# Optimization experiments

Measured on AMD Instinct MI355X. Metric: run time of the kernel, lower is better.

The kernel has to match this reference:

```python
import jax, jax.numpy as jnp
import numpy as np


def _rotate_half(t):
    t1, t2 = jnp.split(t, 2, axis=-1)
    return jnp.concatenate([-t2, t1], axis=-1)


def setup_inputs() -> dict:
    key = jax.random.key(0)
    ks = jax.random.split(key, 6)
    B, N, C, H = 4, 2048, 1024, 16
    D = C // H
    N_ROPE = N - 4  # prefix of 4 tokens skips RoPE
    return {
        "x": jax.random.normal(ks[0], (B, N, C), dtype=jnp.float32),
        "sin": jax.random.normal(ks[1], (N_ROPE, D), dtype=jnp.float32),
        "cos": jax.random.normal(ks[2], (N_ROPE, D), dtype=jnp.float32),
        "w_qkv": jax.random.normal(ks[3], (3 * C, C), dtype=jnp.float32) * (C ** -0.5),
        "w_proj": jax.random.normal(ks[4], (C, C), dtype=jnp.float32) * (C ** -0.5),
        "b_proj": jax.random.normal(ks[5], (C,), dtype=jnp.float32) * 0.02,
    }


def reference(x, sin, cos, w_qkv, w_proj, b_proj):
    B, N, C = x.shape
    H = 16
    D = C // H
    # QKV projection (no bias): [B,N,3C] -> [B,N,3,H,D]
    qkv = jnp.einsum("bnc,fc->bnf", x, w_qkv).reshape(B, N, 3, H, D)
    q, k, v = (jnp.transpose(qkv[:, :, i], (0, 2, 1, 3)) for i in range(3))  # [B,H,N,D]
    # RoPE on suffix tokens only (prefix = N - rope_len)
    prefix = N - sin.shape[-2]
    q_s, k_s = q[:, :, prefix:, :], k[:, :, prefix:, :]
    q = jnp.concatenate([q[:, :, :prefix, :], q_s * cos + _rotate_half(q_s) * sin], axis=2)
    k = jnp.concatenate([k[:, :, :prefix, :], k_s * cos + _rotate_half(k_s) * sin], axis=2)
    # Scaled dot-product attention
    scale = 1.0 / jnp.sqrt(jnp.asarray(D, dtype=q.dtype))
    attn = jax.nn.softmax(jnp.einsum("bhqd,bhkd->bhqk", q, k) * scale, axis=-1)
    o = jnp.einsum("bhqk,bhkd->bhqd", attn, v)
    o = jnp.transpose(o, (0, 2, 1, 3)).reshape(B, N, C)
    return jnp.einsum("bnc,oc->bno", o, w_proj) + b_proj
```

## Files before the change

### kernel.cpp

```cpp
#include <hip/hip_runtime.h>
#include <stdint.h>

typedef __bf16 bf16x8 __attribute__((ext_vector_type(8)));
typedef _Float16 f16x8 __attribute__((ext_vector_type(8)));
typedef float f32x4 __attribute__((ext_vector_type(4)));
typedef short s16x8 __attribute__((ext_vector_type(8)));
typedef short s16x4 __attribute__((ext_vector_type(4)));
typedef unsigned int u32x4 __attribute__((ext_vector_type(4)));

__device__ __forceinline__ unsigned short f2bf(float f) {
  unsigned u = __builtin_bit_cast(unsigned, f);
  u += 0x7fff + ((u >> 16) & 1);
  return (unsigned short)(u >> 16);
}
__device__ __forceinline__ unsigned short f2h(float f) {
  return __builtin_bit_cast(unsigned short, (_Float16)f);
}
__device__ __forceinline__ float exp2i(float x) {
  float r;
  asm("v_exp_f32 %0, %1" : "=v"(r) : "v"(x));
  return r;
}
__device__ __forceinline__ float max3f(float a, float b, float c) {
  float r;
  asm("v_max3_f32 %0, %1, %2, %3" : "=v"(r) : "v"(a), "v"(b), "v"(c));
  return r;
}
__device__ __forceinline__ unsigned cvtpkh(float lo, float hi) {
  auto r = __builtin_amdgcn_cvt_pkrtz(lo, hi);
  return __builtin_bit_cast(unsigned, r);
}

__device__ __forceinline__ void gload_lds16(const void* g, void* l) {
  __builtin_amdgcn_global_load_lds(
      (const __attribute__((address_space(1))) unsigned int*)g,
      (__attribute__((address_space(3))) unsigned int*)l, 16, 0, 0);
}

__device__ __forceinline__ f32x4 mfma_bf(bf16x8 a, bf16x8 b, f32x4 c) {
  return __builtin_amdgcn_mfma_f32_16x16x32_bf16(a, b, c, 0, 0, 0);
}
__device__ __forceinline__ f32x4 mfma_h(f16x8 a, f16x8 b, f32x4 c) {
  return __builtin_amdgcn_mfma_f32_16x16x32_f16(a, b, c, 0, 0, 0);
}
__device__ __forceinline__ bf16x8 bc8(s16x8 v) { return __builtin_bit_cast(bf16x8, v); }
__device__ __forceinline__ f16x8 hc8(s16x8 v) { return __builtin_bit_cast(f16x8, v); }

__global__ void k_cvt_all(const float* __restrict__ x, const float* __restrict__ wq,
                          const float* __restrict__ wp,
                          unsigned short* __restrict__ xb,
                          unsigned short* __restrict__ wqb,
                          unsigned short* __restrict__ wpb) {
  int i = blockIdx.x * blockDim.x + threadIdx.x;
  const float* in; unsigned short* out; int j = i;
  if (i < 2097152)        { in = x;  out = xb;  }
  else if (i < 2883584)   { in = wq; out = wqb; j = i - 2097152; }
  else                    { in = wp; out = wpb; j = i - 2883584; }
  float4 v = ((const float4*)in)[j];
  ushort4 o;
  o.x = f2bf(v.x); o.y = f2bf(v.y); o.z = f2bf(v.z); o.w = f2bf(v.w);
  ((ushort4*)out)[j] = o;
}

__global__ __launch_bounds__(256) void k_gemm_qkv(
    const unsigned short* __restrict__ A, const unsigned short* __restrict__ Bm,
    unsigned short* __restrict__ Qf, unsigned short* __restrict__ Kf,
    unsigned short* __restrict__ Vb,
    const float* __restrict__ sin_t, const float* __restrict__ cos_t) {
  const int M_K = 1024;
  __shared__ unsigned short As[128 * 64];
  __shared__ unsigned short Bs[128 * 64];
  const int tid = threadIdx.x;
  const int lane = tid & 63;
  const int l15 = lane & 15, g = lane >> 4;
  const int wid = tid >> 6, wr = wid >> 1, wc = wid & 1;
  const int lid = blockIdx.y * 24 + blockIdx.x;
  const int swz = (lid & 7) * 192 + (lid >> 3);
  const int by = swz / 24, bx = swz - by * 24;
  const long m0 = (long)by * 128, n0 = (long)bx * 128;

  const int srow = tid >> 3, scu = tid & 7, sc = scu ^ (srow & 7);
  f32x4 acc[4][4] = {};

  for (int k0 = 0; k0 < M_K; k0 += 64) {
#pragma unroll
    for (int p = 0; p < 4; ++p) {
      int u = p * 256 + tid;
      int row = srow + p * 32;
      gload_lds16(A + (m0 + row) * M_K + k0 + sc * 8, (char*)As + u * 16);
      gload_lds16(Bm + (n0 + row) * M_K + k0 + sc * 8, (char*)Bs + u * 16);
    }
    __syncthreads();
    bf16x8 af[4][2], bfr[4][2];
#pragma unroll
    for (int i = 0; i < 4; ++i) {
#pragma unroll
      for (int kk = 0; kk < 2; ++kk) {
        int ua = ((kk * 4 + g) ^ (l15 & 7));
        af[i][kk]  = bc8(*(const s16x8*)&As[(wr * 64 + i * 16 + l15) * 64 + ua * 8]);
        bfr[i][kk] = bc8(*(const s16x8*)&Bs[(wc * 64 + i * 16 + l15) * 64 + ua * 8]);
      }
    }
#pragma unroll
    for (int mi = 0; mi < 4; ++mi)
#pragma unroll
      for (int ni = 0; ni < 4; ++ni) {
        acc[mi][ni] = mfma_bf(af[mi][0], bfr[ni][0], acc[mi][ni]);
        acc[mi][ni] = mfma_bf(af[mi][1], bfr[ni][1], acc[mi][ni]);
      }
    __syncthreads();
  }

  const int colbase = (int)n0 + wc * 64;
  const int s  = colbase >> 10;
  const int h  = (colbase >> 6) & 15;
  const float QSC = 0.125f * 1.44269504089f;
#pragma unroll
  for (int mi = 0; mi < 4; ++mi)
#pragma unroll
    for (int r = 0; r < 4; ++r) {
      long m = m0 + wr * 64 + mi * 16 + g * 4 + r;
      int b = (int)(m >> 11), n = (int)(m & 2047);
      long slab = ((long)(b * 16 + h)) * 131072 + (long)n * 64;
      float v0 = acc[mi][0][r], v1 = acc[mi][1][r];
      float v2 = acc[mi][2][r], v3 = acc[mi][3][r];
      if (s == 2) {
        Vb[slab + l15]      = f2h(v0);
        Vb[slab + 16 + l15] = f2h(v1);
        Vb[slab + 32 + l15] = f2h(v2);
        Vb[slab + 48 + l15] = f2h(v3);
      } else {
        float o0 = v0, o1 = v1, o2 = v2, o3 = v3;
        if (n >= 4) {
          const float* cs = cos_t + (long)(n - 4) * 64;
          const float* sn = sin_t + (long)(n - 4) * 64;
          float c0 = cs[l15], c1 = cs[16 + l15], c2 = cs[32 + l15], c3 = cs[48 + l15];
          float s0 = sn[l15], s1 = sn[16 + l15], s2 = sn[32 + l15], s3 = sn[48 + l15];
          float t0 = o0, t1 = o1;
          o0 = o0 * c0 - o2 * s0;  o1 = o1 * c1 - o3 * s1;
          o2 = o2 * c2 + t0 * s2;  o3 = o3 * c3 + t1 * s3;
        }
        if (s == 0) { o0 *= QSC; o1 *= QSC; o2 *= QSC; o3 *= QSC; }
        unsigned short* H = (s == 0) ? Qf : Kf;
        H[slab + l15]      = f2h(o0);
        H[slab + 16 + l15] = f2h(o1);
        H[slab + 32 + l15] = f2h(o2);
        H[slab + 48 + l15] = f2h(o3);
      }
    }
}

__global__ __launch_bounds__(256) void k_vtrans(const unsigned short* __restrict__ Vb,
                                                unsigned short* __restrict__ Vt) {
  __shared__ unsigned short T[64 * 256];
  const int tid = threadIdx.x;
  const int bh = blockIdx.y;
  const int n0 = blockIdx.x * 256;
  const long slab = (long)bh * 131072;
#pragma unroll
  for (int it = 0; it < 8; ++it) {
    int u = it * 256 + tid;
    int key = u >> 3, dc = u & 7;
    s16x8 v = *(const s16x8*)&Vb[slab + (long)(n0 + key) * 64 + dc * 8];
#pragma unroll
    for (int i = 0; i < 8; ++i) {
      int d = dc * 8 + i;
      T[d * 256 + (key ^ (dc << 3))] = (unsigned short)v[i];
    }
  }
  __syncthreads();
#pragma unroll
  for (int it = 0; it < 8; ++it) {
    int w = it * 256 + tid;
    int d = w >> 5, uc = w & 31;
    int tile = uc >> 3, unit = uc & 7;
    int hh = unit >> 2, gg = unit & 3;
    int ka = tile * 64 + hh * 16 + gg * 4;
    int dc = d >> 3;
    s16x4 a = *(const s16x4*)&T[d * 256 + (ka ^ (dc << 3))];
    s16x4 b = *(const s16x4*)&T[d * 256 + ((ka + 32) ^ (dc << 3))];
    s16x8 v = {a[0], a[1], a[2], a[3], b[0], b[1], b[2], b[3]};
    *(s16x8*)&Vt[slab + (long)d * 2048 + n0 + uc * 8] = v;
  }
}

__global__ __launch_bounds__(256) void k_gemm_proj(
    const unsigned short* __restrict__ A, const unsigned short* __restrict__ Bm,
    float* __restrict__ Cf, const float* __restrict__ bias, int M, int N, int K) {
  __shared__ unsigned short As[128 * 64];
  __shared__ unsigned short Bs[128 * 64];
  const int tid = threadIdx.x;
  const int lane = tid & 63;
  const int l15 = lane & 15, g = lane >> 4;
  const int wid = tid >> 6, wr = wid >> 1, wc = wid & 1;
  const int lid = blockIdx.y * 8 + blockIdx.x;
  const int swz = (lid & 7) * 64 + (lid >> 3);
  const int by = swz >> 3, bx = swz & 7;
  const long m0 = (long)by * 128, n0 = (long)bx * 128;

  const int srow = tid >> 3, scu = tid & 7, sc = scu ^ (srow & 7);
  f32x4 acc[4][4] = {};

  for (int k0 = 0; k0 < K; k0 += 64) {
#pragma unroll
    for (int p = 0; p < 4; ++p) {
      int u = p * 256 + tid;
      int row = srow + p * 32;
      gload_lds16(A + (m0 + row) * K + k0 + sc * 8, (char*)As + u * 16);
      gload_lds16(Bm + (n0 + row) * K + k0 + sc * 8, (char*)Bs + u * 16);
    }
    __syncthreads();
    bf16x8 af[4][2], bfr[4][2];
#pragma unroll
    for (int i = 0; i < 4; ++i) {
#pragma unroll
      for (int kk = 0; kk < 2; ++kk) {
        int ua = ((kk * 4 + g) ^ (l15 & 7));
        af[i][kk]  = bc8(*(const s16x8*)&As[(wr * 64 + i * 16 + l15) * 64 + ua * 8]);
        bfr[i][kk] = bc8(*(const s16x8*)&Bs[(wc * 64 + i * 16 + l15) * 64 + ua * 8]);
      }
    }
#pragma unroll
    for (int mi = 0; mi < 4; ++mi)
#pragma unroll
      for (int ni = 0; ni < 4; ++ni) {
        acc[mi][ni] = mfma_bf(af[mi][0], bfr[ni][0], acc[mi][ni]);
        acc[mi][ni] = mfma_bf(af[mi][1], bfr[ni][1], acc[mi][ni]);
      }
    __syncthreads();
  }

#pragma unroll
  for (int mi = 0; mi < 4; ++mi)
#pragma unroll
    for (int ni = 0; ni < 4; ++ni) {
      long col = n0 + wc * 64 + ni * 16 + l15;
#pragma unroll
      for (int r = 0; r < 4; ++r) {
        long row = m0 + wr * 64 + mi * 16 + g * 4 + r;
        Cf[row * N + col] = acc[mi][ni][r] + bias[col];
      }
    }
}

__global__ __launch_bounds__(256) void k_flash(
    const unsigned short* __restrict__ Qf, const unsigned short* __restrict__ Kf,
    const unsigned short* __restrict__ Vt, unsigned short* __restrict__ o) {
  __shared__ unsigned short KS[2][128 * 64];
  __shared__ unsigned short VtS[2][64 * 128];
  const int tid = threadIdx.x;
  const int lane = tid & 63, wid = tid >> 6;
  const int l15 = lane & 15, g = lane >> 4;
  const int j = blockIdx.x;
  const int c = j & 7, s = j >> 3;
  const int bh = ((s >> 4) << 3) | c;
  const int qt = s & 15;
  const int b = bh >> 4, h = bh & 15;
  const int q0 = qt * 128 + wid * 32;
  const long slab = (long)bh * 131072;

  const long qrowA = slab + (long)(q0 + l15) * 64;
  const long qrowB = slab + (long)(q0 + 16 + l15) * 64;
  f16x8 qa0 = hc8(*(const s16x8*)&Qf[qrowA + g * 8]);
  f16x8 qa1 = hc8(*(const s16x8*)&Qf[qrowA + 32 + g * 8]);
  f16x8 qb0 = hc8(*(const s16x8*)&Qf[qrowB + g * 8]);
  f16x8 qb1 = hc8(*(const s16x8*)&Qf[qrowB + 32 + g * 8]);

  const u32x4 ones_raw = {0x3c003c00u, 0x3c003c00u, 0x3c003c00u, 0x3c003c00u};
  const f16x8 ones = __builtin_bit_cast(f16x8, ones_raw);

  f32x4 ova[4] = {}, ovb[4] = {};
  f32x4 lacA = {}, lacB = {};
  float mrunA = -1e30f, mrunB = -1e30f;

  const int cK = (tid & 7) ^ ((tid >> 3) & 7);
  const int cV = (tid & 7) ^ ((tid >> 4) & 7);
  const int ktV = (tid >> 3) & 1;
  const unsigned short* kSrc = Kf + slab + (long)(tid >> 3) * 64 + cK * 8;
  const unsigned short* vSrc = Vt + slab + (long)(tid >> 4) * 2048 + ktV * 64 + cV * 8;

  auto stage = [&](int buf) {
#pragma unroll
    for (int p = 0; p < 4; ++p) {
      gload_lds16(kSrc + p * 2048,  (char*)&KS[buf][0]  + (p * 256 + tid) * 16);
      gload_lds16(vSrc + p * 32768, (char*)&VtS[buf][0] + (p * 256 + tid) * 16);
    }
    kSrc += 8192;
    vSrc += 128;
  };

  stage(0);
  __syncthreads();

  for (int t = 0; t < 16; ++t) {
    const int cur = t & 1;
    if (t < 15) stage(cur ^ 1);

    f32x4 sa[8], sb[8];
    __builtin_amdgcn_s_setprio(1);
#pragma unroll
    for (int kt = 0; kt < 8; ++kt) {
      f32x4 xa = {}, xb = {};
#pragma unroll
      for (int kk = 0; kk < 2; ++kk) {
        int row = kt * 16 + l15;
        int uu = row * 8 + ((kk * 4 + g) ^ (row & 7));
        f16x8 kf = hc8(*(const s16x8*)&KS[cur][uu * 8]);
        xa = mfma_h(kf, kk ? qa1 : qa0, xa);
        xb = mfma_h(kf, kk ? qb1 : qb0, xb);
      }
      sa[kt] = xa; sb[kt] = xb;
    }
    __builtin_amdgcn_s_setprio(0);

    float ta = fmaxf(sa[0][0], sa[0][1]);
    ta = max3f(ta, sa[0][2], sa[0][3]);
    float tb = fmaxf(sb[0][0], sb[0][1]);
    tb = max3f(tb, sb[0][2], sb[0][3]);
#pragma unroll
    for (int kt = 1; kt < 8; ++kt) {
      ta = max3f(ta, sa[kt][0], sa[kt][1]);
      ta = max3f(ta, sa[kt][2], sa[kt][3]);
      tb = max3f(tb, sb[kt][0], sb[kt][1]);
      tb = max3f(tb, sb[kt][2], sb[kt][3]);
    }
    ta = fmaxf(ta, __shfl_xor(ta, 16)); ta = fmaxf(ta, __shfl_xor(ta, 32));
    tb = fmaxf(tb, __shfl_xor(tb, 16)); tb = fmaxf(tb, __shfl_xor(tb, 32));

    if (!__all(ta <= mrunA + 8.f && tb <= mrunB + 8.f)) {
      float mA = fmaxf(mrunA, ta), mB = fmaxf(mrunB, tb);
      float cA = exp2i(mrunA - mA), cB = exp2i(mrunB - mB);
      lacA *= cA; lacB *= cB;
#pragma unroll
      for (int dt = 0; dt < 4; ++dt) { ova[dt] *= cA; ovb[dt] *= cB; }
      mrunA = mA; mrunB = mB;
    }

    unsigned pa[8][2], pbv[8][2];
#pragma unroll
    for (int kt = 0; kt < 8; ++kt) {
      float a0 = exp2i(sa[kt][0] - mrunA), a1 = exp2i(sa[kt][1] - mrunA);
      float a2 = exp2i(sa[kt][2] - mrunA), a3 = exp2i(sa[kt][3] - mrunA);
      float b0 = exp2i(sb[kt][0] - mrunB), b1 = exp2i(sb[kt][1] - mrunB);
      float b2 = exp2i(sb[kt][2] - mrunB), b3 = exp2i(sb[kt][3] - mrunB);
      pa[kt][0]  = cvtpkh(a0, a1); pa[kt][1]  = cvtpkh(a2, a3);
      pbv[kt][0] = cvtpkh(b0, b1); pbv[kt][1] = cvtpkh(b2, b3);
    }

    __builtin_amdgcn_s_setprio(1);
#pragma unroll
    for (int ktile = 0; ktile < 2; ++ktile) {
      int kb = ktile * 4;
#pragma unroll
      for (int h2 = 0; h2 < 2; ++h2) {
        u32x4 brawA = {pa[kb + h2][0], pa[kb + h2][1],
                       pa[kb + h2 + 2][0], pa[kb + h2 + 2][1]};
        u32x4 brawB = {pbv[kb + h2][0], pbv[kb + h2][1],
                       pbv[kb + h2 + 2][0], pbv[kb + h2 + 2][1]};
        f16x8 pfA = __builtin_bit_cast(f16x8, brawA);
        f16x8 pfB = __builtin_bit_cast(f16x8, brawB);
        lacA = mfma_h(ones, pfA, lacA);
        lacB = mfma_h(ones, pfB, lacB);
#pragma unroll
        for (int dt = 0; dt < 4; ++dt) {
          int d = dt * 16 + l15;
          int vv = d * 16 + ktile * 8 + ((h2 * 4 + g) ^ (d & 7));
          f16x8 vf = hc8(*(const s16x8*)&VtS[cur][vv * 8]);
          ova[dt] = mfma_h(vf, pfA, ova[dt]);
          ovb[dt] = mfma_h(vf, pfB, ovb[dt]);
        }
      }
    }
    __builtin_amdgcn_s_setprio(0);
    __syncthreads();
  }

  float rA = 1.0f / lacA[0], rB = 1.0f / lacB[0];
  long orowA = ((long)(b * 2048 + q0 + l15)) * 1024 + h * 64;
  long orowB = ((long)(b * 2048 + q0 + 16 + l15)) * 1024 + h * 64;
#pragma unroll
  for (int dt = 0; dt < 4; ++dt) {
    ushort4 wa, wb;
    wa.x = f2bf(ova[dt][0] * rA); wa.y = f2bf(ova[dt][1] * rA);
    wa.z = f2bf(ova[dt][2] * rA); wa.w = f2bf(ova[dt][3] * rA);
    wb.x = f2bf(ovb[dt][0] * rB); wb.y = f2bf(ovb[dt][1] * rB);
    wb.z = f2bf(ovb[dt][2] * rB); wb.w = f2bf(ovb[dt][3] * rB);
    *(ushort4*)&o[orowA + dt * 16 + g * 4] = wa;
    *(ushort4*)&o[orowB + dt * 16 + g * 4] = wb;
  }
}

extern "C" void kernel_launch(void* const* d_in, const int* in_sizes, int n_in,
                              void* d_out, int out_size, void* d_ws, size_t ws_size,
                              hipStream_t stream) {
  const float* x      = (const float*)d_in[0];
  const float* sin_t  = (const float*)d_in[1];
  const float* cos_t  = (const float*)d_in[2];
  const float* w_qkv  = (const float*)d_in[3];
  const float* w_proj = (const float*)d_in[4];
  const float* b_proj = (const float*)d_in[5];
  float* out = (float*)d_out;

  char* ws = (char*)d_ws;
  unsigned short* xb     = (unsigned short*)(ws);
  unsigned short* wqkvb  = (unsigned short*)(ws + (16l << 20));
  unsigned short* wprojb = (unsigned short*)(ws + (22l << 20));
  unsigned short* Qf     = (unsigned short*)(ws + (24l << 20));
  unsigned short* Kf     = (unsigned short*)(ws + (40l << 20));
  unsigned short* Vb     = (unsigned short*)(ws + (56l << 20));
  unsigned short* Vt     = (unsigned short*)(ws + (72l << 20));
  unsigned short* ob     = xb;

  k_cvt_all<<<12288, 256, 0, stream>>>(x, w_qkv, w_proj, xb, wqkvb, wprojb);

  k_gemm_qkv<<<dim3(24, 64), 256, 0, stream>>>(xb, wqkvb, Qf, Kf, Vb,
                                               sin_t, cos_t);
  k_vtrans<<<dim3(8, 64), 256, 0, stream>>>(Vb, Vt);
  k_flash<<<dim3(1024), 256, 0, stream>>>(Qf, Kf, Vt, ob);
  k_gemm_proj<<<dim3(8, 64), 256, 0, stream>>>(ob, wprojb, out, b_proj,
                                               8192, 1024, 1024);
}
```

Before: 221.0 us.

## Load V fragments directly from global into registers, drop V LDS staging

Removes the double-buffered V tile from shared memory in the flash-attention kernel. Each wave now loads its V MFMA fragments straight from global memory into registers, issued around the QK^T phase, and sets launch bounds to three blocks per CU. This halves LDS usage and removes LDS reads for V so more blocks can be resident. The cost is more global/L2 traffic, since every wave reloads V with no cross-wave reuse, plus higher register pressure and exposed load latency.

```diff
diff --git a/kernel.cpp b/kernel.cpp
--- a/kernel.cpp
+++ b/kernel.cpp
@@ -243,11 +243,10 @@
     }
 }
 
-__global__ __launch_bounds__(256) void k_flash(
+__global__ __launch_bounds__(256, 3) void k_flash(
     const unsigned short* __restrict__ Qf, const unsigned short* __restrict__ Kf,
     const unsigned short* __restrict__ Vt, unsigned short* __restrict__ o) {
   __shared__ unsigned short KS[2][128 * 64];
-  __shared__ unsigned short VtS[2][64 * 128];
   const int tid = threadIdx.x;
   const int lane = tid & 63, wid = tid >> 6;
   const int l15 = lane & 15, g = lane >> 4;
@@ -274,27 +273,29 @@
   float mrunA = -1e30f, mrunB = -1e30f;
 
   const int cK = (tid & 7) ^ ((tid >> 3) & 7);
-  const int cV = (tid & 7) ^ ((tid >> 4) & 7);
-  const int ktV = (tid >> 3) & 1;
   const unsigned short* kSrc = Kf + slab + (long)(tid >> 3) * 64 + cK * 8;
-  const unsigned short* vSrc = Vt + slab + (long)(tid >> 4) * 2048 + ktV * 64 + cV * 8;
-
-  auto stage = [&](int buf) {
-#pragma unroll
-    for (int p = 0; p < 4; ++p) {
-      gload_lds16(kSrc + p * 2048,  (char*)&KS[buf][0]  + (p * 256 + tid) * 16);
-      gload_lds16(vSrc + p * 32768, (char*)&VtS[buf][0] + (p * 256 + tid) * 16);
-    }
+  const unsigned short* vBase = Vt + slab + (long)l15 * 2048 + g * 8;
+
+  auto stageK = [&](int buf) {
+#pragma unroll
+    for (int p = 0; p < 4; ++p)
+      gload_lds16(kSrc + p * 2048, (char*)&KS[buf][0] + (p * 256 + tid) * 16);
     kSrc += 8192;
-    vSrc += 128;
   };
 
-  stage(0);
+  stageK(0);
   __syncthreads();
 
   for (int t = 0; t < 16; ++t) {
     const int cur = t & 1;
-    if (t < 15) stage(cur ^ 1);
+    if (t < 15) stageK(cur ^ 1);
+
+    s16x8 vr0[8];
+#pragma unroll
+    for (int h2 = 0; h2 < 2; ++h2)
+#pragma unroll
+      for (int dt = 0; dt < 4; ++dt)
+        vr0[h2 * 4 + dt] = *(const s16x8*)(vBase + dt * 32768 + h2 * 32);
 
     f32x4 sa[8], sb[8];
     __builtin_amdgcn_s_setprio(1);
@@ -312,6 +313,14 @@
       sa[kt] = xa; sb[kt] = xb;
     }
     __builtin_amdgcn_s_setprio(0);
+
+    s16x8 vr1[8];
+#pragma unroll
+    for (int h2 = 0; h2 < 2; ++h2)
+#pragma unroll
+      for (int dt = 0; dt < 4; ++dt)
+        vr1[h2 * 4 + dt] = *(const s16x8*)(vBase + dt * 32768 + 64 + h2 * 32);
+    vBase += 128;
 
     float ta = fmaxf(sa[0][0], sa[0][1]);
     ta = max3f(ta, sa[0][2], sa[0][3]);
@@ -363,9 +372,7 @@
         lacB = mfma_h(ones, pfB, lacB);
 #pragma unroll
         for (int dt = 0; dt < 4; ++dt) {
-          int d = dt * 16 + l15;
-          int vv = d * 16 + ktile * 8 + ((h2 * 4 + g) ^ (d & 7));
-          f16x8 vf = hc8(*(const s16x8*)&VtS[cur][vv * 8]);
+          f16x8 vf = hc8(ktile ? vr1[h2 * 4 + dt] : vr0[h2 * 4 + dt]);
           ova[dt] = mfma_h(vf, pfA, ova[dt]);
           ovb[dt] = mfma_h(vf, pfB, ovb[dt]);
         }
```

After: 428.2 us. 1.94x slower.
